# Kernel tuning notes

Hardware: AMD Instinct MI355X
Metric: run time of the kernel (lower is better)

Reference implementation:

```python
import jax, jax.numpy as jnp
import numpy as np

EMBED_DIM = 768
NUM_HEADS = 12
HEAD_DIM = EMBED_DIM // NUM_HEADS


def setup_inputs() -> dict:
    key = jax.random.key(0)
    ks = jax.random.split(key, 9)
    B, N, C = 4, 2048, EMBED_DIM
    s = 1.0 / np.sqrt(C)
    x = jax.random.normal(ks[0], (B, N, C), dtype=jnp.float32)
    Wq = jax.random.normal(ks[1], (C, C), dtype=jnp.float32) * s
    bq = jnp.zeros((C,), dtype=jnp.float32)
    Wk = jax.random.normal(ks[2], (C, C), dtype=jnp.float32) * s
    bk = jnp.zeros((C,), dtype=jnp.float32)
    Wv = jax.random.normal(ks[3], (C, C), dtype=jnp.float32) * s
    bv = jnp.zeros((C,), dtype=jnp.float32)
    Wo = jax.random.normal(ks[4], (C, C), dtype=jnp.float32) * s
    bo = jnp.zeros((C,), dtype=jnp.float32)
    return {"x": x, "Wq": Wq, "bq": bq, "Wk": Wk, "bk": bk,
            "Wv": Wv, "bv": bv, "Wo": Wo, "bo": bo}


def reference(x, Wq, bq, Wk, bk, Wv, bv, Wo, bo):
    # Dropout in eval mode (identity), matching module.eval().
    B, N, C = x.shape
    H, D = NUM_HEADS, HEAD_DIM
    scale = D ** -0.5

    def split_heads(t):  # [B,N,C] -> [B,H,N,D]
        return t.reshape(B, N, H, D).transpose(0, 2, 1, 3)

    q = split_heads(x @ Wq.T + bq)
    k = split_heads(x @ Wk.T + bk)
    v = split_heads(x @ Wv.T + bv)

    attn = jnp.einsum('bhnd,bhmd->bhnm', q, k) * scale  # [B,H,N,N]
    attn = jax.nn.softmax(attn, axis=-1)
    out = jnp.einsum('bhnm,bhmd->bhnd', attn, v)        # [B,H,N,D]
    out = out.transpose(0, 2, 1, 3).reshape(B, N, C)
    return out @ Wo.T + bo
```

## Files before the change

kernel.cpp:

```cpp
#include <hip/hip_runtime.h>
#include <math.h>

#define CDIM 768
#define NHEADS 12
#define HDIM 64
#define BATCH 4
#define SEQ 2048
#define MTOT (BATCH*SEQ)
#define NQKV (3*CDIM)
#define QROWS 128
#define VTILE 4096

typedef __attribute__((ext_vector_type(8))) short bf16x8;
typedef __attribute__((ext_vector_type(4))) float f32x4;
typedef unsigned short u16;
typedef unsigned int u32;

#define ASYNC16(gsrc, ldst) \
  __builtin_amdgcn_global_load_lds((const __attribute__((address_space(1))) void*)(gsrc), \
                                   (__attribute__((address_space(3))) void*)(ldst), 16, 0, 0)

__device__ inline u16 f2b(float x) {
    unsigned int u = __float_as_uint(x);
    return (u16)((u + 0x7fffu + ((u >> 16) & 1u)) >> 16);
}
__device__ inline u32 prnd(float x) { return __float_as_uint(x) + 0x8000u; }

#define XBLK (MTOT*CDIM/1024)
#define WBLK (CDIM*CDIM/1024)
__global__ __launch_bounds__(256)
void prep_kern(const float* __restrict__ x,
               const float* __restrict__ Wq, const float* __restrict__ Wk,
               const float* __restrict__ Wv, const float* __restrict__ Wo,
               const float* __restrict__ bq, const float* __restrict__ bk,
               const float* __restrict__ bv,
               u16* __restrict__ xb, u16* __restrict__ wqkv, u16* __restrict__ wob,
               float* __restrict__ bcat)
{
    int bx = blockIdx.x, tid = threadIdx.x;
    if (bx < XBLK) {
        int i = (bx * 256 + tid) * 4;
        float4 v = *(const float4*)(x + i);
        ushort4 o;
        o.x = f2b(v.x); o.y = f2b(v.y); o.z = f2b(v.z); o.w = f2b(v.w);
        *(ushort4*)(xb + i) = o;
    } else if (bx < XBLK + 4*WBLK) {
        int z = (bx - XBLK) / WBLK;
        int blk = (bx - XBLK) % WBLK;
        const float* src = (z == 0) ? Wq : (z == 1) ? Wk : (z == 2) ? Wv : Wo;
        u16* dst = (z == 3) ? wob : wqkv + (size_t)z * CDIM * CDIM;
        int i = (blk * 256 + tid) * 4;
        float4 v = *(const float4*)(src + i);
        ushort4 o;
        o.x = f2b(v.x); o.y = f2b(v.y); o.z = f2b(v.z); o.w = f2b(v.w);
        *(ushort4*)(dst + i) = o;
    } else {
        int i = (bx - XBLK - 4*WBLK) * 256 + tid;
        if (i < CDIM) bcat[i] = bq[i];
        else if (i < 2*CDIM) bcat[i] = bk[i - CDIM];
        else if (i < 3*CDIM) bcat[i] = bv[i - 2*CDIM];
    }
}

template<int OUTF32, int VFRAG>
__global__ __launch_bounds__(256)
void gemm_bf16(const u16* __restrict__ A, const u16* __restrict__ B,
               const float* __restrict__ bias, void* __restrict__ Y,
               u16* __restrict__ Vt,
               int N, int K, int qn, float qscale)
{
    __shared__ __align__(16) u16 As[2][128*64];
    __shared__ __align__(16) u16 Bs[2][128*64];
    const int tid = threadIdx.x;
    const int nwg = gridDim.x * gridDim.y;
    const int fid = blockIdx.y * gridDim.x + blockIdx.x;
    const int swz = (fid & 7) * (nwg >> 3) + (fid >> 3);
    const int m0 = (swz / gridDim.x) * 128, n0 = (swz % gridDim.x) * 128;
    const int wid = tid >> 6, lane = tid & 63;
    const int wm = (wid & 1) * 64, wn = (wid >> 1) * 64;
    const int l15 = lane & 15, quad = lane >> 4;

    f32x4 acc[4][4];
    #pragma unroll
    for (int i = 0; i < 4; ++i)
        #pragma unroll
        for (int j = 0; j < 4; ++j)
            #pragma unroll
            for (int r = 0; r < 4; ++r) acc[i][j][r] = 0.f;

    auto stage = [&](int buf, int t) {
        int k0 = t * 64;
        #pragma unroll
        for (int r = 0; r < 4; ++r) {
            int li = r*256 + tid;
            int row = li >> 3, c = li & 7;
            int gc = c ^ (row & 7);
            ASYNC16(A + (size_t)(m0 + row) * K + k0 + gc*8, &As[buf][li*8]);
            ASYNC16(B + (size_t)(n0 + row) * K + k0 + gc*8, &Bs[buf][li*8]);
        }
    };

    const int NT = K / 64;
    stage(0, 0);
    __syncthreads();

    for (int t = 0; t < NT; ++t) {
        const int bufc = t & 1;
        if (t + 1 < NT) stage(bufc ^ 1, t + 1);
        #pragma unroll
        for (int kk = 0; kk < 2; ++kk) {
            bf16x8 a[4], b[4];
            #pragma unroll
            for (int i = 0; i < 4; ++i) {
                int m = wm + i*16 + l15;
                int ca = (kk*4 + quad) ^ (m & 7);
                a[i] = *(const bf16x8*)&As[bufc][m*64 + ca*8];
                int n = wn + i*16 + l15;
                int cbx = (kk*4 + quad) ^ (n & 7);
                b[i] = *(const bf16x8*)&Bs[bufc][n*64 + cbx*8];
            }
            #pragma unroll
            for (int i = 0; i < 4; ++i)
                #pragma unroll
                for (int j = 0; j < 4; ++j)
                    acc[i][j] = __builtin_amdgcn_mfma_f32_16x16x32_bf16(a[i], b[j], acc[i][j], 0, 0, 0);
        }
        __syncthreads();
    }

    if (VFRAG && n0 >= 2*CDIM) {
        #pragma unroll
        for (int i = 0; i < 4; ++i) {
            int gm = m0 + wm + i*16 + quad*4;
            int bb = gm >> 11;
            int kt = (gm & 2047) >> 6;
            int t  = i >> 1;
            int wj = (i & 1) * 4;
            #pragma unroll
            for (int j = 0; j < 4; ++j) {
                int gn = n0 + wn + j*16 + l15;
                float bv = bias[gn];
                int d = gn - 2*CDIM;
                int h = d >> 6, jd = (d & 63) >> 4;
                int bh = bb * NHEADS + h;
                u32 p0 = prnd(acc[i][j][0] + bv);
                u32 p1 = prnd(acc[i][j][1] + bv);
                u32 p2 = prnd(acc[i][j][2] + bv);
                u32 p3 = prnd(acc[i][j][3] + bv);
                uint2 st;
                st.x = __builtin_amdgcn_perm(p1, p0, 0x07060302u);
                st.y = __builtin_amdgcn_perm(p3, p2, 0x07060302u);
                *(uint2*)(Vt + ((size_t)(bh*32 + kt))*VTILE
                             + (size_t)((t*4 + jd)*64 + lane)*8 + wj) = st;
            }
        }
    } else {
        #pragma unroll
        for (int i = 0; i < 4; ++i) {
            #pragma unroll
            for (int j = 0; j < 4; ++j) {
                int gn = n0 + wn + j*16 + l15;
                float bv = bias[gn];
                float sc = (gn < qn) ? qscale : 1.0f;
                #pragma unroll
                for (int r = 0; r < 4; ++r) {
                    int gm = m0 + wm + i*16 + quad*4 + r;
                    float v = (acc[i][j][r] + bv) * sc;
                    if (OUTF32) ((float*)Y)[(size_t)gm * N + gn] = v;
                    else        ((u16*)Y)[(size_t)gm * N + gn] = f2b(v);
                }
            }
        }
    }
}

__global__ __launch_bounds__(256, 3)
void attn_mfma(const u16* __restrict__ QK, const u16* __restrict__ Vt,
               u16* __restrict__ Oa)
{
    __shared__ __align__(16) u16 Ks[2][2][64*64];
    __shared__ __align__(16) u16 Vls[2][2][2048];

    const int tid = threadIdx.x;
    const int wid = tid >> 6, lane = tid & 63;
    const int l15 = lane & 15, quad = lane >> 4;
    const int fid = blockIdx.y * gridDim.x + blockIdx.x;
    const int swz = (fid & 7) * 96 + (fid >> 3);
    const int qt = swz & 15, bh = swz >> 4;
    const int b = bh / NHEADS, h = bh % NHEADS;

    const u16* Qg  = QK + ((size_t)(b*SEQ + qt*QROWS)) * NQKV + h*HDIM;
    const u16* Kg0 = QK + ((size_t)(b*SEQ)) * NQKV + CDIM + h*HDIM;
    const u16* Vg  = Vt + (size_t)bh * 32 * VTILE;

    auto stage2 = [&](int wp, int kt) {
        #pragma unroll
        for (int u = 0; u < 2; ++u) {
            #pragma unroll
            for (int r = 0; r < 2; ++r) {
                int li = r*256 + tid, row = li >> 3, c = li & 7, gc = c ^ (row & 7);
                ASYNC16(Kg0 + (size_t)((kt+u)*64 + row) * NQKV + gc*8, &Ks[wp][u][li*8]);
            }
            ASYNC16(Vg + (size_t)(kt+u) * VTILE + tid*8, &Vls[wp][u][tid*8]);
        }
    };

    stage2(0, 0);

    bf16x8 qf[2][2];
    #pragma unroll
    for (int mb = 0; mb < 2; ++mb)
        #pragma unroll
        for (int kk = 0; kk < 2; ++kk)
            qf[mb][kk] = *(const bf16x8*)(Qg + (size_t)(wid*32 + mb*16 + l15) * NQKV + kk*32 + quad*8);

    const bf16x8 ONES8 = { (short)0x3F80, (short)0x3F80, (short)0x3F80, (short)0x3F80,
                           (short)0x3F80, (short)0x3F80, (short)0x3F80, (short)0x3F80 };
    const f32x4 ZERO4 = { 0.f, 0.f, 0.f, 0.f };

    f32x4 o[2][4];
    #pragma unroll
    for (int mb = 0; mb < 2; ++mb)
        #pragma unroll
        for (int j = 0; j < 4; ++j)
            #pragma unroll
            for (int r = 0; r < 4; ++r) o[mb][j][r] = 0.f;
    f32x4 ll[2];
    #pragma unroll
    for (int mb = 0; mb < 2; ++mb)
        #pragma unroll
        for (int r = 0; r < 4; ++r) ll[mb][r] = 0.f;

    __syncthreads();

    auto body = [&](int kt, int rp, int u) {
        bf16x8 vf[2][4];
        #pragma unroll
        for (int jd = 0; jd < 4; ++jd) {
            vf[0][jd] = *(const bf16x8*)&Vls[rp][u][(size_t)(jd*64 + lane)*8];
            vf[1][jd] = *(const bf16x8*)(Vg + (size_t)kt * VTILE
                                         + (size_t)((4 + jd)*64 + lane)*8);
        }

        f32x4 s[2][4];
        __builtin_amdgcn_s_setprio(1);
        #pragma unroll
        for (int j = 0; j < 4; ++j) {
            int kr = j*16 + l15;
            int ck = quad ^ (kr & 7);
            bf16x8 ak = *(const bf16x8*)&Ks[rp][u][kr*64 + ck*8];
            #pragma unroll
            for (int mb = 0; mb < 2; ++mb)
                s[mb][j] = __builtin_amdgcn_mfma_f32_16x16x32_bf16(ak, qf[mb][0], ZERO4, 0, 0, 0);
        }
        #pragma unroll
        for (int j = 0; j < 4; ++j) {
            int kr = j*16 + l15;
            int ck = (4 + quad) ^ (kr & 7);
            bf16x8 ak = *(const bf16x8*)&Ks[rp][u][kr*64 + ck*8];
            #pragma unroll
            for (int mb = 0; mb < 2; ++mb)
                s[mb][j] = __builtin_amdgcn_mfma_f32_16x16x32_bf16(ak, qf[mb][1], s[mb][j], 0, 0, 0);
        }
        __builtin_amdgcn_s_setprio(0);

        bf16x8 pf[2][2];
        #pragma unroll
        for (int mb = 0; mb < 2; ++mb)
            #pragma unroll
            for (int t = 0; t < 2; ++t) {
                u32 a0 = prnd(__builtin_amdgcn_exp2f(s[mb][2*t][0]));
                u32 a1 = prnd(__builtin_amdgcn_exp2f(s[mb][2*t][1]));
                u32 a2 = prnd(__builtin_amdgcn_exp2f(s[mb][2*t][2]));
                u32 a3 = prnd(__builtin_amdgcn_exp2f(s[mb][2*t][3]));
                u32 b0 = prnd(__builtin_amdgcn_exp2f(s[mb][2*t+1][0]));
                u32 b1 = prnd(__builtin_amdgcn_exp2f(s[mb][2*t+1][1]));
                u32 b2 = prnd(__builtin_amdgcn_exp2f(s[mb][2*t+1][2]));
                u32 b3 = prnd(__builtin_amdgcn_exp2f(s[mb][2*t+1][3]));
                union { uint4 u; bf16x8 v; } cst;
                cst.u.x = __builtin_amdgcn_perm(a1, a0, 0x07060302u);
                cst.u.y = __builtin_amdgcn_perm(a3, a2, 0x07060302u);
                cst.u.z = __builtin_amdgcn_perm(b1, b0, 0x07060302u);
                cst.u.w = __builtin_amdgcn_perm(b3, b2, 0x07060302u);
                pf[mb][t] = cst.v;
            }

        __builtin_amdgcn_s_setprio(1);
        #pragma unroll
        for (int t = 0; t < 2; ++t) {
            #pragma unroll
            for (int jd = 0; jd < 4; ++jd) {
                #pragma unroll
                for (int mb = 0; mb < 2; ++mb)
                    o[mb][jd] = __builtin_amdgcn_mfma_f32_16x16x32_bf16(pf[mb][t], vf[t][jd], o[mb][jd], 0, 0, 0);
            }
            #pragma unroll
            for (int mb = 0; mb < 2; ++mb)
                ll[mb] = __builtin_amdgcn_mfma_f32_16x16x32_bf16(pf[mb][t], ONES8, ll[mb], 0, 0, 0);
        }
        __builtin_amdgcn_s_setprio(0);
    };

    for (int s = 0; s < 16; ++s) {
        const int rp = s & 1, wp = rp ^ 1;
        if (s < 15) stage2(wp, 2*s + 2);
        body(2*s,     rp, 0);
        body(2*s + 1, rp, 1);
        __syncthreads();
    }

    u16* Og = Oa + ((size_t)(b*SEQ + qt*QROWS)) * CDIM + h*HDIM;
    #pragma unroll
    for (int mb = 0; mb < 2; ++mb) {
        #pragma unroll
        for (int r = 0; r < 4; ++r) {
            float inv = 1.f / ll[mb][r];
            int row = wid*32 + mb*16 + quad*4 + r;
            #pragma unroll
            for (int jd = 0; jd < 4; ++jd)
                Og[(size_t)row * CDIM + jd*16 + l15] = f2b(o[mb][jd][r] * inv);
        }
    }
}

extern "C" void kernel_launch(void* const* d_in, const int* in_sizes, int n_in,
                              void* d_out, int out_size, void* d_ws, size_t ws_size,
                              hipStream_t stream)
{
    const float* x  = (const float*)d_in[0];
    const float* Wq = (const float*)d_in[1];
    const float* bq = (const float*)d_in[2];
    const float* Wk = (const float*)d_in[3];
    const float* bk = (const float*)d_in[4];
    const float* Wv = (const float*)d_in[5];
    const float* bv = (const float*)d_in[6];
    const float* Wo = (const float*)d_in[7];
    const float* bo = (const float*)d_in[8];

    unsigned char* ws = (unsigned char*)d_ws;
    u16* xb   = (u16*)ws;  ws += (size_t)MTOT * CDIM * 2;
    u16* wqkv = (u16*)ws;  ws += (size_t)NQKV * CDIM * 2;
    u16* wob  = (u16*)ws;  ws += (size_t)CDIM * CDIM * 2;
    float* bcat = (float*)ws; ws += (size_t)NQKV * 4;
    u16* qkv  = (u16*)ws;  ws += (size_t)MTOT * NQKV * 2;
    u16* vt   = (u16*)ws;  ws += (size_t)BATCH*NHEADS*32*VTILE * 2;
    u16* ao   = (u16*)ws;

    prep_kern<<<XBLK + 4*WBLK + 9, 256, 0, stream>>>(x, Wq, Wk, Wv, Wo, bq, bk, bv,
                                                     xb, wqkv, wob, bcat);

    gemm_bf16<0,1><<<dim3(NQKV/128, MTOT/128), 256, 0, stream>>>(xb, wqkv, bcat, qkv, vt, NQKV, CDIM, CDIM, 0.18033688f);
    attn_mfma<<<dim3(SEQ/QROWS, BATCH*NHEADS), 256, 0, stream>>>(qkv, vt, ao);
    gemm_bf16<1,0><<<dim3(CDIM/128, MTOT/128), 256, 0, stream>>>(ao, wob, bo, (float*)d_out, nullptr, CDIM, CDIM, 0, 1.0f);
}
```

Baseline: 209.6 us.

## Enlarge GEMM tiles to 256x256 with 512 threads and split-K half-stage pipelining

Both projection GEMMs now use 256x256 output tiles with 8 waves of 512 threads, each wave holding an 8x4 grid of MFMA accumulators. The K=64 step is split into two 32-wide halves, each with its own LDS buffer and a new XOR swizzle. Loads for the next half are issued before computing the current one, with explicit vmcnt waits and raw barriers, and s_setprio is raised around the MFMA block. This aims to raise operand reuse and overlap global loads with compute, at the cost of more registers and LDS and far fewer workgroups (e.g. 96 for the output projection), which may underfill the GPU.

```diff
diff --git a/kernel.cpp b/kernel.cpp
--- a/kernel.cpp
+++ b/kernel.cpp
@@ -63,79 +63,95 @@
 }
 
 template<int OUTF32, int VFRAG>
-__global__ __launch_bounds__(256)
+__global__ __launch_bounds__(512)
 void gemm_bf16(const u16* __restrict__ A, const u16* __restrict__ B,
                const float* __restrict__ bias, void* __restrict__ Y,
                u16* __restrict__ Vt,
                int N, int K, int qn, float qscale)
 {
-    __shared__ __align__(16) u16 As[2][128*64];
-    __shared__ __align__(16) u16 Bs[2][128*64];
+    __shared__ __align__(16) u16 As[2][2][256*32];
+    __shared__ __align__(16) u16 Bs[2][2][256*32];
     const int tid = threadIdx.x;
     const int nwg = gridDim.x * gridDim.y;
     const int fid = blockIdx.y * gridDim.x + blockIdx.x;
     const int swz = (fid & 7) * (nwg >> 3) + (fid >> 3);
-    const int m0 = (swz / gridDim.x) * 128, n0 = (swz % gridDim.x) * 128;
+    const int m0 = (swz / gridDim.x) * 256, n0 = (swz % gridDim.x) * 256;
     const int wid = tid >> 6, lane = tid & 63;
-    const int wm = (wid & 1) * 64, wn = (wid >> 1) * 64;
+    const int wm = (wid & 1) * 128, wn = (wid >> 1) * 64;
     const int l15 = lane & 15, quad = lane >> 4;
 
-    f32x4 acc[4][4];
-    #pragma unroll
-    for (int i = 0; i < 4; ++i)
+    f32x4 acc[8][4];
+    #pragma unroll
+    for (int i = 0; i < 8; ++i)
         #pragma unroll
         for (int j = 0; j < 4; ++j)
             #pragma unroll
             for (int r = 0; r < 4; ++r) acc[i][j][r] = 0.f;
 
-    auto stage = [&](int buf, int t) {
-        int k0 = t * 64;
-        #pragma unroll
-        for (int r = 0; r < 4; ++r) {
-            int li = r*256 + tid;
-            int row = li >> 3, c = li & 7;
-            int gc = c ^ (row & 7);
-            ASYNC16(A + (size_t)(m0 + row) * K + k0 + gc*8, &As[buf][li*8]);
-            ASYNC16(B + (size_t)(n0 + row) * K + k0 + gc*8, &Bs[buf][li*8]);
+    auto stageK = [&](int buf, int t, int kk) {
+        int k0 = t * 64 + kk * 32;
+        #pragma unroll
+        for (int r = 0; r < 2; ++r) {
+            int li = r*512 + tid;
+            int row = li >> 2, c = li & 3;
+            int gc = c ^ ((row >> 1) & 3);
+            ASYNC16(A + (size_t)(m0 + row) * K + k0 + gc*8, &As[buf][kk][li*8]);
+            ASYNC16(B + (size_t)(n0 + row) * K + k0 + gc*8, &Bs[buf][kk][li*8]);
         }
     };
 
+    auto compute_kk = [&](int buf, int kk) {
+        bf16x8 a[8], b[4];
+        #pragma unroll
+        for (int i = 0; i < 8; ++i) {
+            int m = wm + i*16 + l15;
+            int ca = quad ^ ((m >> 1) & 3);
+            a[i] = *(const bf16x8*)&As[buf][kk][m*32 + ca*8];
+        }
+        #pragma unroll
+        for (int j = 0; j < 4; ++j) {
+            int n = wn + j*16 + l15;
+            int cb = quad ^ ((n >> 1) & 3);
+            b[j] = *(const bf16x8*)&Bs[buf][kk][n*32 + cb*8];
+        }
+        __builtin_amdgcn_s_setprio(1);
+        #pragma unroll
+        for (int i = 0; i < 8; ++i)
+            #pragma unroll
+            for (int j = 0; j < 4; ++j)
+                acc[i][j] = __builtin_amdgcn_mfma_f32_16x16x32_bf16(a[i], b[j], acc[i][j], 0, 0, 0);
+        __builtin_amdgcn_s_setprio(0);
+    };
+
     const int NT = K / 64;
-    stage(0, 0);
-    __syncthreads();
+    stageK(0, 0, 0);
+    stageK(0, 0, 1);
+    asm volatile("s_waitcnt vmcnt(4)" ::: "memory");
+    __builtin_amdgcn_s_barrier();
 
     for (int t = 0; t < NT; ++t) {
-        const int bufc = t & 1;
-        if (t + 1 < NT) stage(bufc ^ 1, t + 1);
-        #pragma unroll
-        for (int kk = 0; kk < 2; ++kk) {
-            bf16x8 a[4], b[4];
-            #pragma unroll
-            for (int i = 0; i < 4; ++i) {
-                int m = wm + i*16 + l15;
-                int ca = (kk*4 + quad) ^ (m & 7);
-                a[i] = *(const bf16x8*)&As[bufc][m*64 + ca*8];
-                int n = wn + i*16 + l15;
-                int cbx = (kk*4 + quad) ^ (n & 7);
-                b[i] = *(const bf16x8*)&Bs[bufc][n*64 + cbx*8];
-            }
-            #pragma unroll
-            for (int i = 0; i < 4; ++i)
-                #pragma unroll
-                for (int j = 0; j < 4; ++j)
-                    acc[i][j] = __builtin_amdgcn_mfma_f32_16x16x32_bf16(a[i], b[j], acc[i][j], 0, 0, 0);
-        }
-        __syncthreads();
+        const int bufc = t & 1, bufn = bufc ^ 1;
+        const bool more = (t + 1 < NT);
+        if (more) stageK(bufn, t + 1, 0);
+        compute_kk(bufc, 0);
+        if (more) asm volatile("s_waitcnt vmcnt(4)" ::: "memory");
+        else      asm volatile("s_waitcnt vmcnt(0)" ::: "memory");
+        __builtin_amdgcn_s_barrier();
+        if (more) stageK(bufn, t + 1, 1);
+        compute_kk(bufc, 1);
+        if (more) asm volatile("s_waitcnt vmcnt(4)" ::: "memory");
+        else      asm volatile("s_waitcnt vmcnt(0)" ::: "memory");
+        __builtin_amdgcn_s_barrier();
     }
 
     if (VFRAG && n0 >= 2*CDIM) {
         #pragma unroll
-        for (int i = 0; i < 4; ++i) {
+        for (int i = 0; i < 8; ++i) {
             int gm = m0 + wm + i*16 + quad*4;
             int bb = gm >> 11;
             int kt = (gm & 2047) >> 6;
-            int t  = i >> 1;
-            int wj = (i & 1) * 4;
+            int t  = (gm >> 5) & 1;
+            int wj = ((gm >> 4) & 1) * 4;
             #pragma unroll
             for (int j = 0; j < 4; ++j) {
                 int gn = n0 + wn + j*16 + l15;
@@ -156,7 +172,7 @@
         }
     } else {
         #pragma unroll
-        for (int i = 0; i < 4; ++i) {
+        for (int i = 0; i < 8; ++i) {
             #pragma unroll
             for (int j = 0; j < 4; ++j) {
                 int gn = n0 + wn + j*16 + l15;
@@ -349,7 +365,7 @@
     prep_kern<<<XBLK + 4*WBLK + 9, 256, 0, stream>>>(x, Wq, Wk, Wv, Wo, bq, bk, bv,
                                                      xb, wqkv, wob, bcat);
 
-    gemm_bf16<0,1><<<dim3(NQKV/128, MTOT/128), 256, 0, stream>>>(xb, wqkv, bcat, qkv, vt, NQKV, CDIM, CDIM, 0.18033688f);
+    gemm_bf16<0,1><<<dim3(NQKV/256, MTOT/256), 512, 0, stream>>>(xb, wqkv, bcat, qkv, vt, NQKV, CDIM, CDIM, 0.18033688f);
     attn_mfma<<<dim3(SEQ/QROWS, BATCH*NHEADS), 256, 0, stream>>>(qkv, vt, ao);
-    gemm_bf16<1,0><<<dim3(CDIM/128, MTOT/128), 256, 0, stream>>>(ao, wob, bo, (float*)d_out, nullptr, CDIM, CDIM, 0, 1.0f);
-}
+    gemm_bf16<1,0><<<dim3(CDIM/256, MTOT/256), 512, 0, stream>>>(ao, wob, bo, (float*)d_out, nullptr, CDIM, CDIM, 0, 1.0f);
+}
```

Measured after the change: 241.4 us. 1.15x slower.
